# Kernel optimization log

Measured on AMD Instinct MI355X. Metric: run time of the kernel, lower is better.

The kernel has to match this reference:

```python
import jax, jax.numpy as jnp
import numpy as np
from jax import lax

DN = ('NCHW', 'OIHW', 'NCHW')


def setup_inputs() -> dict:
    key = jax.random.key(0)
    k1, k2, k3 = jax.random.split(key, 3)
    x = jax.random.normal(k1, (8, 16, 256, 256), dtype=jnp.float32)
    w_perceive = jax.random.normal(k2, (128, 16, 3, 3), dtype=jnp.float32) * 0.02
    w_update = jax.random.normal(k3, (16, 128, 1, 1), dtype=jnp.float32) * 0.01
    return {"x": x, "w_perceive": w_perceive, "w_update": w_update, "steps": 64}


def reference(x, w_perceive, w_update, steps):
    def step(h, _):
        # perceive: 3x3 conv, 16 -> 128 channels, SAME padding, no bias
        p = lax.conv_general_dilated(h, w_perceive, (1, 1), 'SAME', dimension_numbers=DN)
        # update: ReLU then 1x1 conv, 128 -> 16 channels, no bias
        dx = lax.conv_general_dilated(jax.nn.relu(p), w_update, (1, 1), 'SAME', dimension_numbers=DN)
        h = h + dx
        # clamp alive channel to [0,1], hidden channels to [-3,3]
        h = jnp.concatenate([
            jnp.clip(h[:, 0:1], 0.0, 1.0),
            jnp.clip(h[:, 1:], -3.0, 3.0),
        ], axis=1)
        return h, None

    x, _ = lax.scan(step, x, None, length=steps)
    return x
```

## Files before the change

kernel.cpp:

```cpp
#include <hip/hip_runtime.h>
#include <hip/hip_bf16.h>

#define NSTEPS 64

typedef __attribute__((ext_vector_type(8))) short bf16x8;
typedef __attribute__((ext_vector_type(4))) float f32x4;

static __device__ __forceinline__ unsigned int cvtpk_bf16(float lo, float hi) {
  unsigned int d;
  asm("v_cvt_pk_bf16_f32 %0, %1, %2" : "=v"(d) : "v"(lo), "v"(hi));
  return d;
}

static __device__ __forceinline__ bf16x8 gload16(const __hip_bfloat16* p) {
  bf16x8 r;
  asm volatile("global_load_dwordx4 %0, %1, off" : "=v"(r) : "v"(p));
  return r;
}

__global__ void ca_prep(const float* __restrict__ w1, const float* __restrict__ w2,
                        __hip_bfloat16* __restrict__ fr) {
  int i = blockIdx.x * 256 + threadIdx.x;
  if (i < 20480) {
    int j  = i & 7;
    int l  = (i >> 3) & 63;
    int fi = i >> 9;
    int kc = fi % 5, mb = fi / 5;
    int m  = l & 15;
    int co = ((mb >> 1) << 5) + ((m >> 2) << 3) + ((mb & 1) << 2) + (m & 3);
    int k  = kc * 32 + ((l >> 4) << 3) + j;
    float v = 0.0f;
    if (k < 144) {
      int tap = k >> 4, ci = k & 15;
      v = w1[(co * 16 + ci) * 9 + tap];
    }
    fr[i] = __float2bfloat16(v);
  } else if (i < 22528) {
    int i2  = i - 20480;
    int j   = i2 & 7;
    int l   = (i2 >> 3) & 63;
    int kc2 = i2 >> 9;
    int k2  = kc2 * 32 + ((l >> 4) << 3) + j;
    fr[i] = __float2bfloat16(w2[(l & 15) * 128 + k2]);
  }
}

#define TILE0 16384
#define TILE1 21568

template <bool IN_NCHW, bool OUT_NCHW>
__launch_bounds__(256, 2)
__global__ void ca_step(const float* __restrict__ hin,
                        float* __restrict__ hout,
                        const __hip_bfloat16* __restrict__ fr) {
  __shared__ __align__(16) char smem[26752];
  const int tid  = threadIdx.x;
  const int lane = tid & 63;
  const int w    = tid >> 6;
  const int bid  = blockIdx.x;
  const int b    = bid & 7;
  const int t    = bid >> 3;
  const int ty   = t >> 4;
  const int tx   = t & 15;
  const int Y0   = ty << 4, X0 = tx << 4;
  const int ib   = b << 20;

  bf16x8 a1r[2][5];
#pragma unroll
  for (int ml = 0; ml < 2; ++ml)
#pragma unroll
    for (int kc = 0; kc < 5; ++kc) {
      const int mb = (w << 1) + ml;
      a1r[ml][kc] = gload16(fr + (((mb * 5 + kc) * 64 + lane) << 3));
    }
  bf16x8 w2f[4];
#pragma unroll
  for (int kc = 0; kc < 4; ++kc)
    w2f[kc] = gload16(fr + 20480 + ((kc * 64 + lane) << 3));
  asm volatile("s_waitcnt vmcnt(0)" ::: "memory");

  for (int i = tid; i < 18 * 18; i += 256) {
    int y  = i / 18;
    int x  = i - y * 18;
    int GY = Y0 + y - 1, GX = X0 + x - 1;
    bool inb = ((unsigned)GY < 256u) && ((unsigned)GX < 256u);
    unsigned int pk[8];
    if (IN_NCHW) {
      int gof = ib + (GY << 8) + GX;
#pragma unroll
      for (int c = 0; c < 8; ++c) {
        float v0 = inb ? hin[gof + ((2 * c) << 16)] : 0.0f;
        float v1 = inb ? hin[gof + ((2 * c + 1) << 16)] : 0.0f;
        pk[c] = cvtpk_bf16(v0, v1);
      }
    } else {
      f32x4 q[4];
      if (inb) {
        const f32x4* rp = (const f32x4*)(hin + ib + (GY << 12) + (GX << 4));
#pragma unroll
        for (int qq = 0; qq < 4; ++qq) q[qq] = rp[qq];
      } else {
        const f32x4 z = {0.0f, 0.0f, 0.0f, 0.0f};
#pragma unroll
        for (int qq = 0; qq < 4; ++qq) q[qq] = z;
      }
#pragma unroll
      for (int c = 0; c < 8; ++c)
        pk[c] = cvtpk_bf16(q[c >> 1][(c & 1) * 2], q[c >> 1][(c & 1) * 2 + 1]);
    }
    *(uint4*)(smem + TILE0 + i * 16) = make_uint4(pk[0], pk[1], pk[2], pk[3]);
    *(uint4*)(smem + TILE1 + i * 16) = make_uint4(pk[4], pk[5], pk[6], pk[7]);
  }
  __syncthreads();

  const int pix     = lane & 15;
  const int g       = lane >> 4;
  const int g1b     = g >> 1;
  const int halfoff = (g & 1) ? TILE1 : TILE0;

  const f32x4 z4 = {0.0f, 0.0f, 0.0f, 0.0f};

#pragma unroll 1
  for (int j = 0; j < 4; ++j) {
    const int py = Y0 + 4 * j + w;
    float hv[4];
    if (IN_NCHW) {
      const int gbB = ib + (py << 8) + X0 + pix;
#pragma unroll
      for (int r = 0; r < 4; ++r)
        hv[r] = hin[gbB + (((g << 2) + r) << 16)];
    } else {
      const f32x4 hvv =
          *(const f32x4*)(hin + ib + (py << 12) + ((X0 + pix) << 4) + (g << 2));
#pragma unroll
      for (int r = 0; r < 4; ++r) hv[r] = hvv[r];
    }

    f32x4 acc[4][2];
#pragma unroll
    for (int i = 0; i < 4; ++i)
#pragma unroll
      for (int ml = 0; ml < 2; ++ml) acc[i][ml] = z4;

#pragma unroll
    for (int kc = 0; kc < 5; ++kc) {
      const int t0   = 2 * kc;
      const int t1   = (2 * kc + 1 > 8) ? 8 : 2 * kc + 1;
      const int off0 = ((t0 / 3) * 18 + (t0 % 3)) * 16;
      const int off1 = ((t1 / 3) * 18 + (t1 % 3)) * 16;
#pragma unroll
      for (int i = 0; i < 4; ++i) {
        const char* rowbase = smem + halfoff + ((4 * j + i) * 18 + pix) * 16;
        const bf16x8 b1 = *(const bf16x8*)(rowbase + (g1b ? off1 : off0));
#pragma unroll
        for (int ml = 0; ml < 2; ++ml)
          acc[i][ml] = __builtin_amdgcn_mfma_f32_16x16x32_bf16(a1r[ml][kc], b1,
                                                               acc[i][ml], 0, 0, 0);
      }
    }

#pragma unroll
    for (int i = 0; i < 4; ++i) {
      union { unsigned int u[4]; bf16x8 v; } bb;
      bb.u[0] = cvtpk_bf16(fmaxf(acc[i][0][0], 0.0f), fmaxf(acc[i][0][1], 0.0f));
      bb.u[1] = cvtpk_bf16(fmaxf(acc[i][0][2], 0.0f), fmaxf(acc[i][0][3], 0.0f));
      bb.u[2] = cvtpk_bf16(fmaxf(acc[i][1][0], 0.0f), fmaxf(acc[i][1][1], 0.0f));
      bb.u[3] = cvtpk_bf16(fmaxf(acc[i][1][2], 0.0f), fmaxf(acc[i][1][3], 0.0f));
      *(bf16x8*)(smem + (i << 12) + (w << 10) + (lane << 4)) = bb.v;
    }
    __syncthreads();

    f32x4 dxa = z4;
    const char* bs = smem + (w << 12) + (lane << 4);
#pragma unroll
    for (int kc2 = 0; kc2 < 4; ++kc2) {
      const bf16x8 b2 = *(const bf16x8*)(bs + (kc2 << 10));
      dxa = __builtin_amdgcn_mfma_f32_16x16x32_bf16(w2f[kc2], b2, dxa, 0, 0, 0);
    }

    if (OUT_NCHW) {
      const int gbo = ib + (py << 8) + X0 + pix;
#pragma unroll
      for (int r = 0; r < 4; ++r) {
        const int co2 = (g << 2) + r;
        float v = hv[r] + dxa[r];
        const float lo = (co2 == 0) ? 0.0f : -3.0f;
        const float hi = (co2 == 0) ? 1.0f : 3.0f;
        v = fminf(fmaxf(v, lo), hi);
        hout[gbo + (co2 << 16)] = v;
      }
    } else {
      f32x4 ov;
#pragma unroll
      for (int r = 0; r < 4; ++r) {
        const int co2 = (g << 2) + r;
        float v = hv[r] + dxa[r];
        const float lo = (co2 == 0) ? 0.0f : -3.0f;
        const float hi = (co2 == 0) ? 1.0f : 3.0f;
        ov[r] = fminf(fmaxf(v, lo), hi);
      }
      *(f32x4*)(hout + ib + (py << 12) + ((X0 + pix) << 4) + (g << 2)) = ov;
    }
    __syncthreads();
  }
}

extern "C" void kernel_launch(void* const* d_in, const int* in_sizes, int n_in,
                              void* d_out, int out_size, void* d_ws, size_t ws_size,
                              hipStream_t stream) {
  const float* x  = (const float*)d_in[0];
  const float* w1 = (const float*)d_in[1];
  const float* w2 = (const float*)d_in[2];
  float* out  = (float*)d_out;
  float* ping = (float*)d_ws;
  __hip_bfloat16* fr = (__hip_bfloat16*)((char*)d_ws + 33554432);

  ca_prep<<<88, 256, 0, stream>>>(w1, w2, fr);

  for (int s = 0; s < NSTEPS; ++s) {
    const float* in = (s == 0) ? x : ((s & 1) ? ping : out);
    float* o        = (s & 1) ? out : ping;
    if (s == 0)
      ca_step<true, false><<<2048, 256, 0, stream>>>(in, o, fr);
    else if (s == NSTEPS - 1)
      ca_step<false, true><<<2048, 256, 0, stream>>>(in, o, fr);
    else
      ca_step<false, false><<<2048, 256, 0, stream>>>(in, o, fr);
  }
}
```

Measured before the change: 1.703 ms.

## Give each wave all 128 hidden channels to keep intermediate in registers

The work split changes so each wave computes all 128 perceive channels for one pixel row instead of 32 channels for four rows. The ReLU output then feeds the second MFMA straight from registers, with no LDS round trip, and the two per-iteration barriers go away. Shared memory shrinks to just the input tile. The cost is that every wave holds the full set of first-layer weight fragments in registers (40 bf16x8 instead of 10), which raises VGPR pressure and may hurt occupancy under launch_bounds(256,2). It also relies on the 16x16 MFMA output layout matching the B-operand layout expected by the second MFMA.

```diff
diff --git a/kernel.cpp b/kernel.cpp
--- a/kernel.cpp
+++ b/kernel.cpp
@@ -45,15 +45,15 @@
   }
 }
 
-#define TILE0 16384
-#define TILE1 21568
+#define TILE0 0
+#define TILE1 5184
 
 template <bool IN_NCHW, bool OUT_NCHW>
 __launch_bounds__(256, 2)
 __global__ void ca_step(const float* __restrict__ hin,
                         float* __restrict__ hout,
                         const __hip_bfloat16* __restrict__ fr) {
-  __shared__ __align__(16) char smem[26752];
+  __shared__ __align__(16) char smem[10368];
   const int tid  = threadIdx.x;
   const int lane = tid & 63;
   const int w    = tid >> 6;
@@ -65,14 +65,12 @@
   const int Y0   = ty << 4, X0 = tx << 4;
   const int ib   = b << 20;
 
-  bf16x8 a1r[2][5];
-#pragma unroll
-  for (int ml = 0; ml < 2; ++ml)
-#pragma unroll
-    for (int kc = 0; kc < 5; ++kc) {
-      const int mb = (w << 1) + ml;
-      a1r[ml][kc] = gload16(fr + (((mb * 5 + kc) * 64 + lane) << 3));
-    }
+  bf16x8 a1r[8][5];
+#pragma unroll
+  for (int mb = 0; mb < 8; ++mb)
+#pragma unroll
+    for (int kc = 0; kc < 5; ++kc)
+      a1r[mb][kc] = gload16(fr + (((mb * 5 + kc) * 64 + lane) << 3));
   bf16x8 w2f[4];
 #pragma unroll
   for (int kc = 0; kc < 4; ++kc)
@@ -121,8 +119,10 @@
   const f32x4 z4 = {0.0f, 0.0f, 0.0f, 0.0f};
 
 #pragma unroll 1
-  for (int j = 0; j < 4; ++j) {
-    const int py = Y0 + 4 * j + w;
+  for (int i = 0; i < 4; ++i) {
+    const int row = (w << 2) + i;
+    const int py  = Y0 + row;
+
     float hv[4];
     if (IN_NCHW) {
       const int gbB = ib + (py << 8) + X0 + pix;
@@ -136,46 +136,34 @@
       for (int r = 0; r < 4; ++r) hv[r] = hvv[r];
     }
 
-    f32x4 acc[4][2];
-#pragma unroll
-    for (int i = 0; i < 4; ++i)
-#pragma unroll
-      for (int ml = 0; ml < 2; ++ml) acc[i][ml] = z4;
-
+    f32x4 acc[8];
+#pragma unroll
+    for (int mb = 0; mb < 8; ++mb) acc[mb] = z4;
+
+    const char* rowbase = smem + halfoff + (row * 18 + pix) * 16;
 #pragma unroll
     for (int kc = 0; kc < 5; ++kc) {
       const int t0   = 2 * kc;
       const int t1   = (2 * kc + 1 > 8) ? 8 : 2 * kc + 1;
       const int off0 = ((t0 / 3) * 18 + (t0 % 3)) * 16;
       const int off1 = ((t1 / 3) * 18 + (t1 % 3)) * 16;
-#pragma unroll
-      for (int i = 0; i < 4; ++i) {
-        const char* rowbase = smem + halfoff + ((4 * j + i) * 18 + pix) * 16;
-        const bf16x8 b1 = *(const bf16x8*)(rowbase + (g1b ? off1 : off0));
-#pragma unroll
-        for (int ml = 0; ml < 2; ++ml)
-          acc[i][ml] = __builtin_amdgcn_mfma_f32_16x16x32_bf16(a1r[ml][kc], b1,
-                                                               acc[i][ml], 0, 0, 0);
-      }
-    }
-
-#pragma unroll
-    for (int i = 0; i < 4; ++i) {
+      const bf16x8 b1 = *(const bf16x8*)(rowbase + (g1b ? off1 : off0));
+#pragma unroll
+      for (int mb = 0; mb < 8; ++mb)
+        acc[mb] = __builtin_amdgcn_mfma_f32_16x16x32_bf16(a1r[mb][kc], b1,
+                                                          acc[mb], 0, 0, 0);
+    }
+
+    f32x4 dxa = z4;
+#pragma unroll
+    for (int q = 0; q < 4; ++q) {
+      const int me = 2 * q, mo = 2 * q + 1;
       union { unsigned int u[4]; bf16x8 v; } bb;
-      bb.u[0] = cvtpk_bf16(fmaxf(acc[i][0][0], 0.0f), fmaxf(acc[i][0][1], 0.0f));
-      bb.u[1] = cvtpk_bf16(fmaxf(acc[i][0][2], 0.0f), fmaxf(acc[i][0][3], 0.0f));
-      bb.u[2] = cvtpk_bf16(fmaxf(acc[i][1][0], 0.0f), fmaxf(acc[i][1][1], 0.0f));
-      bb.u[3] = cvtpk_bf16(fmaxf(acc[i][1][2], 0.0f), fmaxf(acc[i][1][3], 0.0f));
-      *(bf16x8*)(smem + (i << 12) + (w << 10) + (lane << 4)) = bb.v;
-    }
-    __syncthreads();
-
-    f32x4 dxa = z4;
-    const char* bs = smem + (w << 12) + (lane << 4);
-#pragma unroll
-    for (int kc2 = 0; kc2 < 4; ++kc2) {
-      const bf16x8 b2 = *(const bf16x8*)(bs + (kc2 << 10));
-      dxa = __builtin_amdgcn_mfma_f32_16x16x32_bf16(w2f[kc2], b2, dxa, 0, 0, 0);
+      bb.u[0] = cvtpk_bf16(fmaxf(acc[me][0], 0.0f), fmaxf(acc[me][1], 0.0f));
+      bb.u[1] = cvtpk_bf16(fmaxf(acc[me][2], 0.0f), fmaxf(acc[me][3], 0.0f));
+      bb.u[2] = cvtpk_bf16(fmaxf(acc[mo][0], 0.0f), fmaxf(acc[mo][1], 0.0f));
+      bb.u[3] = cvtpk_bf16(fmaxf(acc[mo][2], 0.0f), fmaxf(acc[mo][3], 0.0f));
+      dxa = __builtin_amdgcn_mfma_f32_16x16x32_bf16(w2f[q], bb.v, dxa, 0, 0, 0);
     }
 
     if (OUT_NCHW) {
@@ -201,7 +189,6 @@
       }
       *(f32x4*)(hout + ib + (py << 12) + ((X0 + pix) << 4) + (g << 2)) = ov;
     }
-    __syncthreads();
   }
 }
 
```

Result: slower. 1.983 ms (+16.4%).
